# Kernel tuning notes

Measured on AMD Instinct MI355X. Metric: run time of the kernel, lower is better.

## Reference

```python
import jax, jax.numpy as jnp
import numpy as np

B, K, D = 8, 256, 768      # batch, num proposals, appearance_feature_dim
DK = 96                    # key_feature_dim
DG = 96                    # geo_feature_dim
NR = 8                     # n_relations (NR*DK == D required by residual add)


def setup_inputs() -> dict:
    key = jax.random.key(0)
    ks = jax.random.split(key, 10)
    s = 0.02
    return {
        "f_a": jax.random.normal(ks[0], (B, K, D), jnp.float32),
        "position_embedding": jax.random.uniform(ks[1], (B, K, K, DG), jnp.float32),
        # stacked per-head parameters (NR heads)
        "WG_w": jax.random.normal(ks[2], (NR, DG), jnp.float32) * s,
        "WG_b": jnp.zeros((NR,), jnp.float32),
        "WK_w": jax.random.normal(ks[3], (NR, D, DK), jnp.float32) * s,
        "WK_b": jnp.zeros((NR, DK), jnp.float32),
        "WQ_w": jax.random.normal(ks[4], (NR, D, DK), jnp.float32) * s,
        "WQ_b": jnp.zeros((NR, DK), jnp.float32),
        "WV_w": jax.random.normal(ks[5], (NR, D, DK), jnp.float32) * s,
        "WV_b": jnp.zeros((NR, DK), jnp.float32),
    }


def reference(f_a, position_embedding, WG_w, WG_b, WK_w, WK_b, WQ_w, WQ_b, WV_w, WV_b):
    # Per-head projections, all heads at once: [B, H, K, DK]
    k = jnp.einsum('bkd,hde->bhke', f_a, WK_w) + WK_b[:, None, :]
    q = jnp.einsum('bkd,hde->bhke', f_a, WQ_w) + WQ_b[:, None, :]
    v = jnp.einsum('bkd,hde->bhke', f_a, WV_w) + WV_b[:, None, :]
    # scaled_dot[b,h,m,n] = <k_m, q_n> / sqrt(DK)  (matches w_k.view(B,K,1,dk)*w_q.view(B,1,K,dk))
    scores = jnp.einsum('bhme,bhne->bhmn', k, q) * (1.0 / np.sqrt(DK)).astype(np.float32)
    # geometric bias: relu(WG(pe)) -> [B,H,K,K]
    w_g = jax.nn.relu(jnp.einsum('bmng,hg->bhmn', position_embedding, WG_w) + WG_b[:, None, None])
    logits = jnp.log(jnp.clip(w_g, 1e-6)) + scores
    # torch Softmax(dim=1) on [B,K,K] -> normalize over m axis (axis=2 here)
    attn = jax.nn.softmax(logits, axis=2)
    # output[b,n,:] = sum_m attn[b,h,m,n] * v[b,h,m,:], heads concatenated on feature dim
    out = jnp.einsum('bhmn,bhmd->bnhd', attn, v).reshape(f_a.shape[0], f_a.shape[1], -1)
    return out + f_a  # concat + f_a residual from RelationalProposalModule
```

## Files before the change

kernel.cpp:

```cpp
#include <hip/hip_runtime.h>

#define DD   768
#define NH   8
#define DKh  96

typedef __attribute__((ext_vector_type(8))) short short8;
typedef __attribute__((ext_vector_type(4))) float f32x4;

__device__ __forceinline__ unsigned short f2bf(float x) {
    union { float f; unsigned int u; } v; v.f = x;
    unsigned int r = v.u + 0x7FFFu + ((v.u >> 16) & 1u);
    return (unsigned short)(r >> 16);
}

__global__ __launch_bounds__(256) void k_cvt(const float* __restrict__ fa,
                                             unsigned short* __restrict__ abf,
                                             const float* __restrict__ wk,
                                             const float* __restrict__ wq,
                                             const float* __restrict__ wv,
                                             unsigned short* __restrict__ wbf) {
    __shared__ float ls[64 * 97];
    int bid = blockIdx.x;
    int t = threadIdx.x;
    if (bid < 1536) {
        int idx = bid * 256 + t;
        float4 v = ((const float4*)fa)[idx];
        ushort4 o;
        o.x = f2bf(v.x); o.y = f2bf(v.y); o.z = f2bf(v.z); o.w = f2bf(v.w);
        ((ushort4*)abf)[idx] = o;
        return;
    }
    int wb = bid - 1536;
    int pid = wb / 12;
    int db  = wb % 12;
    int p = pid >> 3, h = pid & 7;
    const float* src = (p == 0 ? wk : p == 1 ? wq : wv) + h * DD * DKh + db * 64 * DKh;
#pragma unroll
    for (int i = 0; i < 24; ++i) {
        int f = t + 256 * i;
        int dl = f / 96, e = f - dl * 96;
        ls[dl * 97 + e] = src[f];
    }
    __syncthreads();
    unsigned short* dst = wbf + (p * 768 + h * 96) * DD + db * 64;
#pragma unroll
    for (int i = 0; i < 24; ++i) {
        int f = t + 256 * i;
        int e = f >> 6, dl = f & 63;
        dst[e * DD + dl] = f2bf(ls[dl * 97 + e]);
    }
}

__global__ __launch_bounds__(256) void k_proj(const unsigned short* __restrict__ abf,
                                              const unsigned short* __restrict__ wbf,
                                              const float* __restrict__ wkb,
                                              const float* __restrict__ wqb,
                                              const float* __restrict__ wvb,
                                              unsigned short* __restrict__ kb,
                                              unsigned short* __restrict__ qb,
                                              unsigned short* __restrict__ vt) {
    int w = threadIdx.x >> 6, lane = threadIdx.x & 63;
    int lrow = lane & 15, quad = lane >> 4;
    int rt = blockIdx.x / 18, cg = blockIdx.x % 18;
    int r0 = rt * 128 + (w >> 1) * 64;
    int c0 = cg * 128 + (w & 1) * 64;
    f32x4 z = {0.f, 0.f, 0.f, 0.f};
    f32x4 acc[4][4] = {{z, z, z, z}, {z, z, z, z}, {z, z, z, z}, {z, z, z, z}};
    for (int kk = 0; kk < DD; kk += 32) {
        short8 a[4], b[4];
#pragma unroll
        for (int i = 0; i < 4; ++i) {
            a[i] = *(const short8*)(abf + (r0 + i * 16 + lrow) * DD + kk + quad * 8);
            b[i] = *(const short8*)(wbf + (c0 + i * 16 + lrow) * DD + kk + quad * 8);
        }
#pragma unroll
        for (int mi = 0; mi < 4; ++mi)
#pragma unroll
            for (int ni = 0; ni < 4; ++ni)
                acc[mi][ni] = __builtin_amdgcn_mfma_f32_16x16x32_bf16(a[mi], b[ni], acc[mi][ni], 0, 0, 0);
    }
#pragma unroll
    for (int mi = 0; mi < 4; ++mi) {
        int rbase = r0 + mi * 16 + quad * 4;
        int b_ = rbase >> 8, mbase = rbase & 255;
#pragma unroll
        for (int ni = 0; ni < 4; ++ni) {
            int cc = c0 + ni * 16 + lrow;
            int p = cc / 768, rm = cc - p * 768;
            int h = rm / 96,  e = rm - h * 96;
            float bias = (p == 0 ? wkb : p == 1 ? wqb : wvb)[h * 96 + e];
            if (p == 2) {
                ushort4 v4;
                v4.x = f2bf(acc[mi][ni][0] + bias);
                v4.y = f2bf(acc[mi][ni][1] + bias);
                v4.z = f2bf(acc[mi][ni][2] + bias);
                v4.w = f2bf(acc[mi][ni][3] + bias);
                *(ushort4*)(vt + ((b_ * 8 + h) * 96 + e) * 256 + mbase) = v4;
            } else {
                float sc = (p == 1) ? 0.10206207261596577f : 1.0f;
                unsigned short* dst = (p == 0 ? kb : qb) + ((b_ * 8 + h) * 256 + mbase) * 96 + e;
#pragma unroll
                for (int r = 0; r < 4; ++r)
                    dst[r * 96] = f2bf((acc[mi][ni][r] + bias) * sc);
            }
        }
    }
}

__global__ __launch_bounds__(256) void k_wgs(const float* __restrict__ pe,
                                             const float* __restrict__ wgw,
                                             const float* __restrict__ wgb,
                                             const unsigned short* __restrict__ kb,
                                             const unsigned short* __restrict__ qb,
                                             float* __restrict__ Lt) {
    __shared__ float stot[8 * 257];
    int bi = blockIdx.x;
    int b = bi >> 8, mt = (bi >> 4) & 15, nt = bi & 15;
    int m0 = mt * 16, n0 = nt * 16;
    int t = threadIdx.x;
    int w = t >> 6, lane = t & 63, lrow = lane & 15, quad = lane >> 4;
    short8 bf[3];
    if (lrow < 8) {
#pragma unroll
        for (int ks = 0; ks < 3; ++ks) {
            const float* wp = wgw + lrow * 96 + ks * 32 + quad * 8;
            float4 w0 = *(const float4*)wp;
            float4 w1 = *(const float4*)(wp + 4);
            short8 bb;
            bb[0] = f2bf(w0.x); bb[1] = f2bf(w0.y); bb[2] = f2bf(w0.z); bb[3] = f2bf(w0.w);
            bb[4] = f2bf(w1.x); bb[5] = f2bf(w1.y); bb[6] = f2bf(w1.z); bb[7] = f2bf(w1.w);
            bf[ks] = bb;
        }
    } else {
        short8 zz8 = {0, 0, 0, 0, 0, 0, 0, 0};
        bf[0] = zz8; bf[1] = zz8; bf[2] = zz8;
    }
    float gbias = wgb[lrow & 7];
    const float* peb0 = pe + (((size_t)b * 256 + m0) * 256 + n0) * 96;
#pragma unroll
    for (int rt4 = 0; rt4 < 4; ++rt4) {
        int rt = w * 4 + rt4;
        int p = rt * 16 + lrow;
        const float* pr = peb0 + (size_t)(p >> 4) * 24576 + (p & 15) * 96;
        f32x4 acc = {0.f, 0.f, 0.f, 0.f};
#pragma unroll
        for (int ks = 0; ks < 3; ++ks) {
            const float* ap = pr + ks * 32 + quad * 8;
            float4 v0 = *(const float4*)ap;
            float4 v1 = *(const float4*)(ap + 4);
            short8 a;
            a[0] = f2bf(v0.x); a[1] = f2bf(v0.y); a[2] = f2bf(v0.z); a[3] = f2bf(v0.w);
            a[4] = f2bf(v1.x); a[5] = f2bf(v1.y); a[6] = f2bf(v1.z); a[7] = f2bf(v1.w);
            acc = __builtin_amdgcn_mfma_f32_16x16x32_bf16(a, bf[ks], acc, 0, 0, 0);
        }
        if (lrow < 8) {
#pragma unroll
            for (int r = 0; r < 4; ++r)
                stot[lrow * 257 + rt * 16 + quad * 4 + r] =
                    __logf(fmaxf(acc[r] + gbias, 1e-6f));
        }
    }
    __syncthreads();
#pragma unroll
    for (int hh = 0; hh < 2; ++hh) {
        int h = w * 2 + hh;
        const unsigned short* ka = kb + ((size_t)((b * 8 + h) * 256) + m0 + lrow) * 96 + quad * 8;
        const unsigned short* qa = qb + ((size_t)((b * 8 + h) * 256) + n0 + lrow) * 96 + quad * 8;
        f32x4 acc = {0.f, 0.f, 0.f, 0.f};
#pragma unroll
        for (int ks = 0; ks < 3; ++ks) {
            short8 a  = *(const short8*)(ka + ks * 32);
            short8 bq = *(const short8*)(qa + ks * 32);
            acc = __builtin_amdgcn_mfma_f32_16x16x32_bf16(a, bq, acc, 0, 0, 0);
        }
        f32x4 ov;
#pragma unroll
        for (int r = 0; r < 4; ++r)
            ov[r] = acc[r] + stot[h * 257 + (quad * 4 + r) * 16 + lrow];
        *(f32x4*)(Lt + ((size_t)((b * 8 + h) * 256) + n0 + lrow) * 256 + m0 + quad * 4) = ov;
    }
}

__global__ __launch_bounds__(256) void k_smv(const float* __restrict__ Lt,
                                             const unsigned short* __restrict__ vt,
                                             const float* __restrict__ fa,
                                             float* __restrict__ out) {
    __shared__ unsigned short P[32 * 264];
    int bid = blockIdx.x;
    int bh = bid >> 3, nt = bid & 7;
    int n0 = nt * 32;
    int t = threadIdx.x, w = t >> 6, lane = t & 63;
    const float* lb = Lt + ((size_t)bh * 256 + n0) * 256;
#pragma unroll
    for (int rr = 0; rr < 8; ++rr) {
        int row = w * 8 + rr;
        float4 v = *((const float4*)(lb + row * 256) + lane);
        float mx = fmaxf(fmaxf(v.x, v.y), fmaxf(v.z, v.w));
#pragma unroll
        for (int d = 1; d < 64; d <<= 1) mx = fmaxf(mx, __shfl_xor(mx, d));
        float e0 = __expf(v.x - mx), e1 = __expf(v.y - mx),
              e2 = __expf(v.z - mx), e3 = __expf(v.w - mx);
        float s = e0 + e1 + e2 + e3;
#pragma unroll
        for (int d = 1; d < 64; d <<= 1) s += __shfl_xor(s, d);
        float inv = 1.0f / s;
        ushort4 o;
        o.x = f2bf(e0 * inv); o.y = f2bf(e1 * inv);
        o.z = f2bf(e2 * inv); o.w = f2bf(e3 * inv);
        *(ushort4*)(P + row * 264 + lane * 4) = o;
    }
    __syncthreads();
    int lrow = lane & 15, quad = lane >> 4;
    int nsub = (w & 1) * 16, eb = (w >> 1) * 48;
    f32x4 zz = {0.f, 0.f, 0.f, 0.f};
    f32x4 acc[3] = {zz, zz, zz};
    const unsigned short* vb = vt + ((size_t)bh * 96 + eb + lrow) * 256 + quad * 8;
    const unsigned short* pb = P + (nsub + lrow) * 264 + quad * 8;
#pragma unroll
    for (int mk = 0; mk < 256; mk += 32) {
        short8 a = *(const short8*)(pb + mk);
#pragma unroll
        for (int tt = 0; tt < 3; ++tt) {
            short8 b = *(const short8*)(vb + tt * 16 * 256 + mk);
            acc[tt] = __builtin_amdgcn_mfma_f32_16x16x32_bf16(a, b, acc[tt], 0, 0, 0);
        }
    }
    int b_ = bh >> 3, h = bh & 7;
#pragma unroll
    for (int tt = 0; tt < 3; ++tt) {
        int idx = (b_ * 256 + n0 + nsub + quad * 4) * 768 + h * 96 + eb + tt * 16 + lrow;
#pragma unroll
        for (int r = 0; r < 4; ++r)
            out[idx + r * 768] = acc[tt][r] + fa[idx + r * 768];
    }
}

extern "C" void kernel_launch(void* const* d_in, const int* in_sizes, int n_in,
                              void* d_out, int out_size, void* d_ws, size_t ws_size,
                              hipStream_t stream) {
    const float* fa  = (const float*)d_in[0];
    const float* pe  = (const float*)d_in[1];
    const float* wgw = (const float*)d_in[2];
    const float* wgb = (const float*)d_in[3];
    const float* wkw = (const float*)d_in[4];
    const float* wkb = (const float*)d_in[5];
    const float* wqw = (const float*)d_in[6];
    const float* wqb = (const float*)d_in[7];
    const float* wvw = (const float*)d_in[8];
    const float* wvb = (const float*)d_in[9];
    float* out = (float*)d_out;
    char* ws = (char*)d_ws;
    unsigned short* abf = (unsigned short*)(ws);
    unsigned short* wbf = (unsigned short*)(ws + 3145728);
    unsigned short* kb  = (unsigned short*)(ws + 6684672);
    unsigned short* qb  = (unsigned short*)(ws + 9830400);
    unsigned short* vt  = (unsigned short*)(ws + 12976128);
    float*          Lt  = (float*)(ws + 16121856);

    k_cvt <<<1824, 256, 0, stream>>>(fa, abf, wkw, wqw, wvw, wbf);
    k_proj<<< 288, 256, 0, stream>>>(abf, wbf, wkb, wqb, wvb, kb, qb, vt);
    k_wgs <<<2048, 256, 0, stream>>>(pe, wgw, wgb, kb, qb, Lt);
    k_smv <<< 512, 256, 0, stream>>>(Lt, vt, fa, out);
}
```

Measured before the change: 372.3 us.

## Move softmax exponent into score kernel and store bf16 unnormalized exps

The score kernel now applies exp with a fixed shift and writes bf16 unnormalized weights instead of fp32 logits, halving the intermediate traffic. The softmax-matmul kernel only sums each row, feeds the bf16 exps directly from global memory into the MFMA, and applies the reciprocal sum at the output. This removes the per-row max pass, the second exp and the shared-memory staging. In exchange it drops the max subtraction, so it relies on logits staying in a bounded range to avoid overflow or underflow.

```diff
diff --git a/kernel.cpp b/kernel.cpp
--- a/kernel.cpp
+++ b/kernel.cpp
@@ -6,11 +6,18 @@
 
 typedef __attribute__((ext_vector_type(8))) short short8;
 typedef __attribute__((ext_vector_type(4))) float f32x4;
+
+#define LOGIT_SHIFT 4.0f
 
 __device__ __forceinline__ unsigned short f2bf(float x) {
     union { float f; unsigned int u; } v; v.f = x;
     unsigned int r = v.u + 0x7FFFu + ((v.u >> 16) & 1u);
     return (unsigned short)(r >> 16);
+}
+
+__device__ __forceinline__ float bf2f(unsigned short u) {
+    union { unsigned int i; float f; } v; v.i = ((unsigned int)u) << 16;
+    return v.f;
 }
 
 __global__ __launch_bounds__(256) void k_cvt(const float* __restrict__ fa,
@@ -112,7 +119,7 @@
                                              const float* __restrict__ wgb,
                                              const unsigned short* __restrict__ kb,
                                              const unsigned short* __restrict__ qb,
-                                             float* __restrict__ Lt) {
+                                             unsigned short* __restrict__ Et) {
     __shared__ float stot[8 * 257];
     int bi = blockIdx.x;
     int b = bi >> 8, mt = (bi >> 4) & 15, nt = bi & 15;
@@ -173,52 +180,44 @@
             short8 bq = *(const short8*)(qa + ks * 32);
             acc = __builtin_amdgcn_mfma_f32_16x16x32_bf16(a, bq, acc, 0, 0, 0);
         }
-        f32x4 ov;
-#pragma unroll
-        for (int r = 0; r < 4; ++r)
-            ov[r] = acc[r] + stot[h * 257 + (quad * 4 + r) * 16 + lrow];
-        *(f32x4*)(Lt + ((size_t)((b * 8 + h) * 256) + n0 + lrow) * 256 + m0 + quad * 4) = ov;
-    }
-}
-
-__global__ __launch_bounds__(256) void k_smv(const float* __restrict__ Lt,
+        ushort4 ev;
+        ev.x = f2bf(__expf(acc[0] + stot[h * 257 + (quad * 4 + 0) * 16 + lrow] - LOGIT_SHIFT));
+        ev.y = f2bf(__expf(acc[1] + stot[h * 257 + (quad * 4 + 1) * 16 + lrow] - LOGIT_SHIFT));
+        ev.z = f2bf(__expf(acc[2] + stot[h * 257 + (quad * 4 + 2) * 16 + lrow] - LOGIT_SHIFT));
+        ev.w = f2bf(__expf(acc[3] + stot[h * 257 + (quad * 4 + 3) * 16 + lrow] - LOGIT_SHIFT));
+        *(ushort4*)(Et + ((size_t)((b * 8 + h) * 256) + n0 + lrow) * 256 + m0 + quad * 4) = ev;
+    }
+}
+
+__global__ __launch_bounds__(256) void k_smv(const unsigned short* __restrict__ Et,
                                              const unsigned short* __restrict__ vt,
                                              const float* __restrict__ fa,
                                              float* __restrict__ out) {
-    __shared__ unsigned short P[32 * 264];
+    __shared__ float inv_s[32];
     int bid = blockIdx.x;
     int bh = bid >> 3, nt = bid & 7;
     int n0 = nt * 32;
     int t = threadIdx.x, w = t >> 6, lane = t & 63;
-    const float* lb = Lt + ((size_t)bh * 256 + n0) * 256;
+    const unsigned short* eb0 = Et + ((size_t)bh * 256 + n0) * 256;
 #pragma unroll
     for (int rr = 0; rr < 8; ++rr) {
         int row = w * 8 + rr;
-        float4 v = *((const float4*)(lb + row * 256) + lane);
-        float mx = fmaxf(fmaxf(v.x, v.y), fmaxf(v.z, v.w));
-#pragma unroll
-        for (int d = 1; d < 64; d <<= 1) mx = fmaxf(mx, __shfl_xor(mx, d));
-        float e0 = __expf(v.x - mx), e1 = __expf(v.y - mx),
-              e2 = __expf(v.z - mx), e3 = __expf(v.w - mx);
-        float s = e0 + e1 + e2 + e3;
+        ushort4 v = *(const ushort4*)(eb0 + row * 256 + lane * 4);
+        float s = bf2f(v.x) + bf2f(v.y) + bf2f(v.z) + bf2f(v.w);
 #pragma unroll
         for (int d = 1; d < 64; d <<= 1) s += __shfl_xor(s, d);
-        float inv = 1.0f / s;
-        ushort4 o;
-        o.x = f2bf(e0 * inv); o.y = f2bf(e1 * inv);
-        o.z = f2bf(e2 * inv); o.w = f2bf(e3 * inv);
-        *(ushort4*)(P + row * 264 + lane * 4) = o;
+        if (lane == 0) inv_s[row] = 1.0f / s;
     }
     __syncthreads();
     int lrow = lane & 15, quad = lane >> 4;
     int nsub = (w & 1) * 16, eb = (w >> 1) * 48;
     f32x4 zz = {0.f, 0.f, 0.f, 0.f};
     f32x4 acc[3] = {zz, zz, zz};
+    const unsigned short* pa = eb0 + (size_t)(nsub + lrow) * 256 + quad * 8;
     const unsigned short* vb = vt + ((size_t)bh * 96 + eb + lrow) * 256 + quad * 8;
-    const unsigned short* pb = P + (nsub + lrow) * 264 + quad * 8;
 #pragma unroll
     for (int mk = 0; mk < 256; mk += 32) {
-        short8 a = *(const short8*)(pb + mk);
+        short8 a = *(const short8*)(pa + mk);
 #pragma unroll
         for (int tt = 0; tt < 3; ++tt) {
             short8 b = *(const short8*)(vb + tt * 16 * 256 + mk);
@@ -231,7 +230,7 @@
         int idx = (b_ * 256 + n0 + nsub + quad * 4) * 768 + h * 96 + eb + tt * 16 + lrow;
 #pragma unroll
         for (int r = 0; r < 4; ++r)
-            out[idx + r * 768] = acc[tt][r] + fa[idx + r * 768];
+            out[idx + r * 768] = acc[tt][r] * inv_s[nsub + quad * 4 + r] + fa[idx + r * 768];
     }
 }
 
@@ -255,10 +254,10 @@
     unsigned short* kb  = (unsigned short*)(ws + 6684672);
     unsigned short* qb  = (unsigned short*)(ws + 9830400);
     unsigned short* vt  = (unsigned short*)(ws + 12976128);
-    float*          Lt  = (float*)(ws + 16121856);
+    unsigned short* Et  = (unsigned short*)(ws + 16121856);
 
     k_cvt <<<1824, 256, 0, stream>>>(fa, abf, wkw, wqw, wvw, wbf);
     k_proj<<< 288, 256, 0, stream>>>(abf, wbf, wkb, wqb, wvb, kb, qb, vt);
-    k_wgs <<<2048, 256, 0, stream>>>(pe, wgw, wgb, kb, qb, Lt);
-    k_smv <<< 512, 256, 0, stream>>>(Lt, vt, fa, out);
-}
+    k_wgs <<<2048, 256, 0, stream>>>(pe, wgw, wgb, kb, qb, Et);
+    k_smv <<< 512, 256, 0, stream>>>(Et, vt, fa, out);
+}
```

Result: no change. 372.4 us (+0.0%).
